# Optimization experiments

Measured on AMD Instinct MI355X. Metric: run time of the kernel, lower is better.

Reference implementation:

```python
import jax, jax.numpy as jnp
import numpy as np

NUM_HEADS = 8      # SD1.x UNet cross-attn heads at 64x64 block
NUM_PROMPTS = 4    # batch = 2*NUM_PROMPTS (uncond + cond CFG halves)


def setup_inputs() -> dict:
    key = jax.random.key(0)
    ks = jax.random.split(key, 8)
    B, T, C = 2 * NUM_PROMPTS, 4096, 320   # spatial tokens, inner dim
    S, D = 77, 768                          # CLIP text seq len / width
    return {
        "hidden_states": jax.random.normal(ks[0], (B, T, C), jnp.float32),
        "encoder_hidden_states": jax.random.normal(ks[1], (B, S, D), jnp.float32),
        "mapper": jax.random.uniform(ks[2], (NUM_PROMPTS - 1, S, S), jnp.float32),
        "Wq": jax.random.normal(ks[3], (C, C), jnp.float32) * 0.02,
        "Wk": jax.random.normal(ks[4], (D, C), jnp.float32) * 0.02,
        "Wv": jax.random.normal(ks[5], (D, C), jnp.float32) * 0.02,
        "Wo": jax.random.normal(ks[6], (C, C), jnp.float32) * 0.02,
        "bo": jnp.zeros((C,), jnp.float32),
    }


def reference(hidden_states, encoder_hidden_states, mapper, Wq, Wk, Wv, Wo, bo):
    B, T, C = hidden_states.shape
    S = encoder_hidden_states.shape[1]
    H = NUM_HEADS
    d = C // H
    scale = 1.0 / jnp.sqrt(jnp.asarray(d, hidden_states.dtype))

    # projections + head split (diffusers head_to_batch_dim layout)
    q = (hidden_states @ Wq).reshape(B, T, H, d)
    k = (encoder_hidden_states @ Wk).reshape(B, S, H, d)
    v = (encoder_hidden_states @ Wv).reshape(B, S, H, d)

    # full attention probabilities must be materialized for the P2P swap
    scores = jnp.einsum('bthd,bshd->bhts', q, k) * scale
    probs = jax.nn.softmax(scores, axis=-1)  # [B, H, T, S]

    # conditional (CFG) half: [P, H, T, S]; swap via mapper einsum (cross-attn,
    # cur_step < num_steps_cross branch of swap_attention_probs)
    half = B // 2
    uncond = probs[:half]
    cond = probs[half:]
    attn_base = cond[0]                                   # [H, T, S]
    replaced = jnp.einsum('htm,pme->phte', attn_base, mapper)  # [P-1, H, T, S]
    cond = jnp.concatenate([attn_base[None], replaced], axis=0)
    probs = jnp.concatenate([uncond, cond], axis=0)

    # value matmul + merge heads (batch_to_head_dim) + output projection
    out = jnp.einsum('bhts,bshd->bthd', probs, v).reshape(B, T, C)
    return out @ Wo + bo
```

## Files before the change

### kernel.cpp

```cpp
#include <hip/hip_runtime.h>
#include <hip/hip_bf16.h>

typedef unsigned short ushort;
typedef __attribute__((ext_vector_type(8))) short bf16x8;
typedef __attribute__((ext_vector_type(8))) unsigned short ushort8;
typedef __attribute__((ext_vector_type(4))) float f32x4;
typedef __attribute__((ext_vector_type(4))) float float4v;

__device__ __forceinline__ ushort f2bf(float f) {
    union { float f; unsigned u; } v; v.f = f;
    unsigned r = v.u + 0x7FFFu + ((v.u >> 16) & 1u);
    return (ushort)(r >> 16);
}
__device__ __forceinline__ float bf2f(ushort u) {
    union { unsigned u; float f; } v; v.u = ((unsigned)u) << 16;
    return v.f;
}

#define QF_SZ   (1280u * 8 * 2 * 512)
#define KF_SZ   (5u * 8 * 5 * 2 * 512)
#define VF_SZ   (5u * 8 * 3 * 3 * 512)
#define VPF_SZ  (3u * 8 * 3 * 3 * 512)
#define WOF_SZ  (10u * 2 * 10 * 512)

__global__ __launch_bounds__(256) void prep_k(
    const float* __restrict__ Wq, const float* __restrict__ Wk,
    const float* __restrict__ Wv, const float* __restrict__ Wo,
    ushort* __restrict__ Wq_t, ushort* __restrict__ Wk_t,
    ushort* __restrict__ Wv_t, ushort* __restrict__ Wo_t,
    ushort* __restrict__ Kf, ushort* __restrict__ Vf, ushort* __restrict__ VPf)
{
    int b = blockIdx.x;
    if (b >= 680) {
        const ushort8 z8 = {0,0,0,0,0,0,0,0};
        unsigned i = (b - 680) * 256 + threadIdx.x;
        if (i < KF_SZ / 8) ((ushort8*)Kf)[i] = z8;
        else if (i < (KF_SZ + VF_SZ) / 8) ((ushort8*)Vf)[i - KF_SZ / 8] = z8;
        else if (i < (KF_SZ + VF_SZ + VPF_SZ) / 8) ((ushort8*)VPf)[i - (KF_SZ + VF_SZ) / 8] = z8;
        return;
    }
    __shared__ ushort t[32][33];
    const float* src; ushort* dst; int K; int tb;
    if (b < 100)      { src = Wq; dst = Wq_t; K = 320; tb = b; }
    else if (b < 340) { src = Wk; dst = Wk_t; K = 768; tb = b - 100; }
    else if (b < 580) { src = Wv; dst = Wv_t; K = 768; tb = b - 340; }
    else              { src = Wo; dst = Wo_t; K = 320; tb = b - 580; }
    int tc = tb % 10, tr = tb / 10;
    int tx = threadIdx.x & 31, ty = threadIdx.x >> 5;
    #pragma unroll
    for (int p = 0; p < 4; ++p) {
        int k = tr * 32 + ty + p * 8, n = tc * 32 + tx;
        t[ty + p * 8][tx] = f2bf(src[(size_t)k * 320 + n]);
    }
    __syncthreads();
    #pragma unroll
    for (int p = 0; p < 4; ++p) {
        int n = tc * 32 + ty + p * 8, k = tr * 32 + tx;
        dst[(size_t)n * K + k] = t[tx][ty + p * 8];
    }
}

__global__ __launch_bounds__(256) void gemm_qkv(
    const float* __restrict__ A, const ushort* __restrict__ Wq_t,
    const float* __restrict__ E, const ushort* __restrict__ Wk_t,
    const ushort* __restrict__ Wv_t, const ushort* __restrict__ Wo_t,
    ushort* __restrict__ Qf, float* __restrict__ part, ushort* __restrict__ Wof)
{
    const int tid = threadIdx.x;
    const int bid = blockIdx.x;
    if (bid >= 480) {
        int i = (bid - 480) * 256 + tid;
        int g = i >> 6, l = i & 63;
        int kk = g / 20, half = (g / 10) & 1, f = g - (g / 10) * 10;
        int n = half * 160 + f * 16 + (l & 15);
        int k0 = kk * 32 + (l >> 4) * 8;
        *(ushort8*)(Wof + (size_t)g * 512 + l * 8) =
            *(const ushort8*)(Wo_t + (size_t)n * 320 + k0);
        return;
    }
    __shared__ ushort A_lds[2][64 * 40];
    __shared__ ushort B_lds[2][320 * 40];
    const int w = tid >> 6, l = tid & 63;
    const int c15 = l & 15, khi = (l >> 4) * 8;
    const int r = tid >> 2, p = (tid & 3) * 8;
    const int rbase = (l >> 4) * 4;
    f32x4 acc[4][5] = {};
    const ushort8 z8 = {0,0,0,0,0,0,0,0};

    if (bid < 160) {
        const int mtile = bid % 10, mat = (bid / 10) & 1, ks = bid / 20;
        const int m0 = mtile * 64, kk0 = ks * 96;
        const ushort* Bt = mat ? Wv_t : Wk_t;
        const int m = m0 + r;
        const bool live = (m < 616);
        const float* Abase = E + (size_t)(live ? m : 0) * 768 + p;
        float4v a0 = {0,0,0,0}, a1 = {0,0,0,0};
        ushort8 breg[5];
        if (live) { a0 = *(const float4v*)(Abase + kk0); a1 = *(const float4v*)(Abase + kk0 + 4); }
        #pragma unroll
        for (int i = 0; i < 5; ++i) {
            int idx = tid + i * 256; int n = idx >> 2, q = (idx & 3) * 8;
            breg[i] = *(const ushort8*)(Bt + (size_t)n * 768 + kk0 + q);
        }
        {
            ushort* d = &A_lds[0][r * 40 + p];
            d[0]=f2bf(a0.x); d[1]=f2bf(a0.y); d[2]=f2bf(a0.z); d[3]=f2bf(a0.w);
            d[4]=f2bf(a1.x); d[5]=f2bf(a1.y); d[6]=f2bf(a1.z); d[7]=f2bf(a1.w);
            #pragma unroll
            for (int i = 0; i < 5; ++i) {
                int idx = tid + i * 256; int n = idx >> 2, q = (idx & 3) * 8;
                *(ushort8*)&B_lds[0][n * 40 + q] = breg[i];
            }
        }
        __syncthreads();
        for (int k = 0; k < 3; ++k) {
            const int cur = k & 1;
            if (k < 2) {
                int kk = kk0 + (k + 1) * 32;
                if (live) { a0 = *(const float4v*)(Abase + kk); a1 = *(const float4v*)(Abase + kk + 4); }
                #pragma unroll
                for (int i = 0; i < 5; ++i) {
                    int idx = tid + i * 256; int n = idx >> 2, q = (idx & 3) * 8;
                    breg[i] = *(const ushort8*)(Bt + (size_t)n * 768 + kk + q);
                }
            }
            bf16x8 a[4];
            #pragma unroll
            for (int mf = 0; mf < 4; ++mf)
                a[mf] = *(const bf16x8*)&A_lds[cur][(mf * 16 + c15) * 40 + khi];
            #pragma unroll
            for (int f = 0; f < 5; ++f) {
                bf16x8 b = *(const bf16x8*)&B_lds[cur][(w * 80 + f * 16 + c15) * 40 + khi];
                #pragma unroll
                for (int mf = 0; mf < 4; ++mf)
                    acc[mf][f] = __builtin_amdgcn_mfma_f32_16x16x32_bf16(a[mf], b, acc[mf][f], 0, 0, 0);
            }
            if (k < 2) {
                const int nxt = cur ^ 1;
                ushort* d = &A_lds[nxt][r * 40 + p];
                d[0]=f2bf(a0.x); d[1]=f2bf(a0.y); d[2]=f2bf(a0.z); d[3]=f2bf(a0.w);
                d[4]=f2bf(a1.x); d[5]=f2bf(a1.y); d[6]=f2bf(a1.z); d[7]=f2bf(a1.w);
                #pragma unroll
                for (int i = 0; i < 5; ++i) {
                    int idx = tid + i * 256; int n = idx >> 2, q = (idx & 3) * 8;
                    *(ushort8*)&B_lds[nxt][n * 40 + q] = breg[i];
                }
                __syncthreads();
            }
        }
        float* dst = part + (size_t)(mat * 8 + ks) * 640 * 320;
        #pragma unroll
        for (int mf = 0; mf < 4; ++mf)
            #pragma unroll
            for (int f = 0; f < 5; ++f) {
                int col = w * 80 + f * 16 + c15;
                #pragma unroll
                for (int rr = 0; rr < 4; ++rr)
                    dst[(size_t)(m0 + mf * 16 + rbase + rr) * 320 + col] = acc[mf][f][rr];
            }
    } else {
        const int m0 = (bid - 160) * 64;
        const float* Abase = A + (size_t)(m0 + r) * 320 + p;
        float4v a0, a1; ushort8 breg[5];
        a0 = *(const float4v*)(Abase + 0);
        a1 = *(const float4v*)(Abase + 4);
        #pragma unroll
        for (int i = 0; i < 5; ++i) {
            int idx = tid + i * 256; int n = idx >> 2, q = (idx & 3) * 8;
            breg[i] = *(const ushort8*)(Wq_t + (size_t)n * 320 + q);
        }
        {
            ushort* d = &A_lds[0][r * 40 + p];
            d[0]=f2bf(a0.x); d[1]=f2bf(a0.y); d[2]=f2bf(a0.z); d[3]=f2bf(a0.w);
            d[4]=f2bf(a1.x); d[5]=f2bf(a1.y); d[6]=f2bf(a1.z); d[7]=f2bf(a1.w);
            #pragma unroll
            for (int i = 0; i < 5; ++i) {
                int idx = tid + i * 256; int n = idx >> 2, q = (idx & 3) * 8;
                *(ushort8*)&B_lds[0][n * 40 + q] = breg[i];
            }
        }
        __syncthreads();
        for (int k = 0; k < 10; ++k) {
            const int cur = k & 1;
            if (k < 9) {
                int kk = (k + 1) * 32;
                a0 = *(const float4v*)(Abase + kk);
                a1 = *(const float4v*)(Abase + kk + 4);
                #pragma unroll
                for (int i = 0; i < 5; ++i) {
                    int idx = tid + i * 256; int n = idx >> 2, q = (idx & 3) * 8;
                    breg[i] = *(const ushort8*)(Wq_t + (size_t)n * 320 + kk + q);
                }
            }
            bf16x8 a[4];
            #pragma unroll
            for (int mf = 0; mf < 4; ++mf)
                a[mf] = *(const bf16x8*)&A_lds[cur][(mf * 16 + c15) * 40 + khi];
            #pragma unroll
            for (int f = 0; f < 5; ++f) {
                bf16x8 b = *(const bf16x8*)&B_lds[cur][(w * 80 + f * 16 + c15) * 40 + khi];
                #pragma unroll
                for (int mf = 0; mf < 4; ++mf)
                    acc[mf][f] = __builtin_amdgcn_mfma_f32_16x16x32_bf16(a[mf], b, acc[mf][f], 0, 0, 0);
            }
            if (k < 9) {
                const int nxt = cur ^ 1;
                ushort* d = &A_lds[nxt][r * 40 + p];
                d[0]=f2bf(a0.x); d[1]=f2bf(a0.y); d[2]=f2bf(a0.z); d[3]=f2bf(a0.w);
                d[4]=f2bf(a1.x); d[5]=f2bf(a1.y); d[6]=f2bf(a1.z); d[7]=f2bf(a1.w);
                #pragma unroll
                for (int i = 0; i < 5; ++i) {
                    int idx = tid + i * 256; int n = idx >> 2, q = (idx & 3) * 8;
                    *(ushort8*)&B_lds[nxt][n * 40 + q] = breg[i];
                }
                __syncthreads();
            }
        }
        const int rg0 = m0 >> 4;
        for (int i = tid; i < 1536; i += 256) {
            int grp = i / 48;
            int lane16 = 16 + (i - grp * 48);
            int rg4 = grp >> 3, h = grp & 7;
            *(ushort8*)(Qf + ((size_t)((rg0 + rg4) * 8 + h) * 2 + 1) * 512 + lane16 * 8) = z8;
        }
        #pragma unroll
        for (int mf = 0; mf < 4; ++mf)
            #pragma unroll
            for (int f = 0; f < 5; ++f) {
                int col = w * 80 + f * 16 + c15;
                int h = col / 40, kd = col - h * 40;
                int kt = kd >> 5, chunk = (kd >> 3) & 3, elem = kd & 7;
                size_t base = ((size_t)((rg0 + mf) * 8 + h) * 2 + kt) * 512;
                #pragma unroll
                for (int rr = 0; rr < 4; ++rr) {
                    int lane = (rbase + rr) | (chunk << 4);
                    Qf[base + lane * 8 + elem] = f2bf(acc[mf][f][rr]);
                }
            }
    }
}

__global__ __launch_bounds__(256) void kv_reduce(
    const float* __restrict__ part, ushort* __restrict__ Kf,
    ushort* __restrict__ Vf, ushort* __restrict__ VVt)
{
    int idx = blockIdx.x * 256 + threadIdx.x;
    if (idx >= 616 * 320) return;
    int mat = blockIdx.y;
    int row = idx / 320, col = idx - row * 320;
    float s8 = 0.f;
    #pragma unroll
    for (int ks = 0; ks < 8; ++ks)
        s8 += part[((size_t)(mat * 8 + ks) * 640 + row) * 320 + col];
    ushort b = f2bf(s8);
    int bt = row / 77, s = row - bt * 77;
    int h = col / 40, kd = col - h * 40;
    if (mat == 0) {
        if (bt < 5) {
            int kt = kd >> 5, chunk = (kd >> 3) & 3;
            int lane = (s & 15) | (chunk << 4);
            Kf[((size_t)((bt * 8 + h) * 5 + (s >> 4)) * 2 + kt) * 512 + lane * 8 + (kd & 7)] = b;
        }
    } else {
        if (bt < 5) {
            int lane = (kd & 15) | (((s >> 3) & 3) << 4);
            Vf[(((size_t)(bt * 8 + h) * 3 + (kd >> 4)) * 3 + (s >> 5)) * 512 + lane * 8 + (s & 7)] = b;
        } else {
            VVt[((size_t)bt * 320 + col) * 80 + s] = b;
        }
    }
}

__global__ void vprime_k(const float* __restrict__ mapper, const ushort* __restrict__ VVt,
                         ushort* __restrict__ VPf)
{
    int pm = blockIdx.x;
    int p = pm / 77, m = pm - p * 77;
    __shared__ float mp[77];
    int tid = threadIdx.x;
    if (tid < 77) mp[tid] = mapper[(size_t)pm * 77 + tid];
    __syncthreads();
    const ushort* vrow = VVt + ((size_t)(5 + p) * 320 + tid) * 80;
    float acc = 0.f;
    for (int e = 0; e < 77; ++e) acc += mp[e] * bf2f(vrow[e]);
    int h = tid / 40, dc = tid - h * 40;
    int lane = (dc & 15) | (((m >> 3) & 3) << 4);
    VPf[(((size_t)(p * 8 + h) * 3 + (dc >> 4)) * 3 + (m >> 5)) * 512 + lane * 8 + (m & 7)] = f2bf(acc);
}

#define ATT_SCALE 0.15811388300841897f
__global__ __launch_bounds__(512, 4) void attn_out_k(
    const ushort* __restrict__ Qf, const ushort* __restrict__ Kf,
    const ushort* __restrict__ Vf, const ushort* __restrict__ VPf,
    const ushort* __restrict__ Wof, const float* __restrict__ bias,
    float* __restrict__ out)
{
    __shared__ __align__(16) ushort AO_lds[64 * 328];
    __shared__ __align__(16) ushort P_lds[8 * 16 * 104];

    const int tid = threadIdx.x;
    const int ww = tid >> 6, l = tid & 63;
    const int rg = ww & 3, half = ww >> 2;
    const int c15 = l & 15, hi4 = l >> 4;
    const int khi = hi4 * 8, rbase = hi4 * 4;
    const int bt = blockIdx.y, t0 = blockIdx.x * 64;
    const int qb = (bt < 5) ? bt : 4;
    const int rowgrp = qb * 256 + blockIdx.x * 4 + rg;
    const ushort* Vfb = (bt < 5) ? (Vf + (size_t)bt * (8 * 3 * 3 * 512))
                                 : (VPf + (size_t)(bt - 5) * (8 * 3 * 3 * 512));
    const ushort8 z8 = {0,0,0,0,0,0,0,0};
    ushort* Pw = P_lds + ww * (16 * 104);

    if (l < 48) {
        int r = l / 3, c = l - 3 * (l / 3);
        *(ushort8*)&Pw[r * 104 + 80 + c * 8] = z8;
    }

    for (int hh = 0; hh < 4; ++hh) {
        const int h = half * 4 + hh;

        bf16x8 qa0 = *(const bf16x8*)(Qf + ((size_t)(rowgrp * 8 + h) * 2 + 0) * 512 + l * 8);
        bf16x8 qa1 = *(const bf16x8*)(Qf + ((size_t)(rowgrp * 8 + h) * 2 + 1) * 512 + l * 8);
        f32x4 sacc[5] = {};
        #pragma unroll
        for (int f = 0; f < 5; ++f) {
            const ushort* kfb = Kf + ((size_t)((qb * 8 + h) * 5 + f) * 2) * 512 + l * 8;
            bf16x8 kb0 = *(const bf16x8*)(kfb);
            bf16x8 kb1 = *(const bf16x8*)(kfb + 512);
            sacc[f] = __builtin_amdgcn_mfma_f32_16x16x32_bf16(qa0, kb0, sacc[f], 0, 0, 0);
            sacc[f] = __builtin_amdgcn_mfma_f32_16x16x32_bf16(qa1, kb1, sacc[f], 0, 0, 0);
        }

        bf16x8 vreg[3][3];
        #pragma unroll
        for (int f = 0; f < 3; ++f)
            #pragma unroll
            for (int kt = 0; kt < 3; ++kt)
                vreg[f][kt] = *(const bf16x8*)(Vfb + (((size_t)(h * 3 + f) * 3 + kt)) * 512 + l * 8);

        float pv[5][4];
        #pragma unroll
        for (int r = 0; r < 4; ++r) {
            float sum = 0.f;
            #pragma unroll
            for (int f = 0; f < 5; ++f) {
                bool valid = (f < 4) || (c15 < 13);
                float e = valid ? __expf(sacc[f][r] * ATT_SCALE) : 0.f;
                pv[f][r] = e; sum += e;
            }
            #pragma unroll
            for (int d = 1; d < 16; d <<= 1) sum += __shfl_xor(sum, d);
            float inv = 1.f / sum;
            #pragma unroll
            for (int f = 0; f < 5; ++f) pv[f][r] *= inv;
        }

        #pragma unroll
        for (int r = 0; r < 4; ++r)
            #pragma unroll
            for (int f = 0; f < 5; ++f)
                Pw[(rbase + r) * 104 + f * 16 + c15] = f2bf(pv[f][r]);

        bf16x8 pa[3];
        #pragma unroll
        for (int kt = 0; kt < 3; ++kt)
            pa[kt] = *(const bf16x8*)&Pw[c15 * 104 + kt * 32 + khi];
        f32x4 oacc[3] = {};
        #pragma unroll
        for (int f = 0; f < 3; ++f)
            #pragma unroll
            for (int kt = 0; kt < 3; ++kt)
                oacc[f] = __builtin_amdgcn_mfma_f32_16x16x32_bf16(pa[kt], vreg[f][kt], oacc[f], 0, 0, 0);
        #pragma unroll
        for (int f = 0; f < 3; ++f) {
            int col = f * 16 + c15;
            if (col < 40) {
                #pragma unroll
                for (int r = 0; r < 4; ++r)
                    AO_lds[(rg * 16 + rbase + r) * 328 + h * 40 + col] = f2bf(oacc[f][r]);
            }
        }
    }
    __syncthreads();

    f32x4 acc[10] = {};
    for (int kk = 0; kk < 10; ++kk) {
        bf16x8 a = *(const bf16x8*)&AO_lds[(rg * 16 + c15) * 328 + kk * 32 + khi];
        const ushort* wb = Wof + (size_t)((kk * 2 + half) * 10) * 512 + l * 8;
        #pragma unroll
        for (int f = 0; f < 10; ++f) {
            bf16x8 b = *(const bf16x8*)(wb + (size_t)f * 512);
            acc[f] = __builtin_amdgcn_mfma_f32_16x16x32_bf16(a, b, acc[f], 0, 0, 0);
        }
    }

    const int cb = half * 160;
    #pragma unroll
    for (int f = 0; f < 10; ++f) {
        int col = cb + f * 16 + c15;
        #pragma unroll
        for (int rr = 0; rr < 4; ++rr)
            out[(size_t)(bt * 4096 + t0 + rg * 16 + rbase + rr) * 320 + col]
                = acc[f][rr] + bias[col];
    }
}

extern "C" void kernel_launch(void* const* d_in, const int* in_sizes, int n_in,
                              void* d_out, int out_size, void* d_ws, size_t ws_size,
                              hipStream_t stream) {
    (void)in_sizes; (void)n_in; (void)out_size; (void)ws_size;
    const float* hs     = (const float*)d_in[0];
    const float* ehs    = (const float*)d_in[1];
    const float* mapper = (const float*)d_in[2];
    const float* Wq     = (const float*)d_in[3];
    const float* Wk     = (const float*)d_in[4];
    const float* Wv     = (const float*)d_in[5];
    const float* Wo     = (const float*)d_in[6];
    const float* bo     = (const float*)d_in[7];
    float* out = (float*)d_out;

    ushort* ws   = (ushort*)d_ws;
    ushort* Wq_t = ws;
    ushort* Wk_t = Wq_t + 320 * 320;
    ushort* Wv_t = Wk_t + 320 * 768;
    ushort* Wo_t = Wv_t + 320 * 768;
    ushort* Wof  = Wo_t + 320 * 320;
    ushort* Qfb  = Wof + WOF_SZ;
    ushort* Kfb  = Qfb + QF_SZ;
    ushort* Vfb  = Kfb + KF_SZ;
    ushort* VPfb = Vfb + VF_SZ;
    ushort* VVt  = VPfb + VPF_SZ;
    float*  part = (float*)(VVt + 8 * 320 * 80);

    prep_k<<<1069, 256, 0, stream>>>(Wq, Wk, Wv, Wo, Wq_t, Wk_t, Wv_t, Wo_t,
                                     Kfb, Vfb, VPfb);
    gemm_qkv<<<530, 256, 0, stream>>>(hs, Wq_t, ehs, Wk_t, Wv_t, Wo_t, Qfb, part, Wof);
    kv_reduce<<<dim3(770, 2), 256, 0, stream>>>(part, Kfb, Vfb, VVt);
    vprime_k<<<231, 320, 0, stream>>>(mapper, VVt, VPfb);
    attn_out_k<<<dim3(64, 8), 512, 0, stream>>>(Qfb, Kfb, Vfb, VPfb, Wof, bo, out);
}
```

Measured before the change: 68.54 us.

## Fuse Q projection into attention kernel, dropping the global Q buffer

The Q projection moves out of the standalone QKV GEMM and into the attention/output kernel. Each block loads its 64 hidden-state rows, converts them to bf16 in LDS, multiplies by a pre-fragmented Wq (Wqf, built alongside Wof), and reads per-head Q fragments straight from LDS. This removes the large write and re-read of Qf through global memory and shrinks the first GEMM launch to K/V only. The cost is recomputing Q for the three cond batches that share batch 4's queries, plus an extra LDS pass and barrier in the attention kernel.

```diff
diff --git a/kernel.cpp b/kernel.cpp
--- a/kernel.cpp
+++ b/kernel.cpp
@@ -17,11 +17,10 @@
     return v.f;
 }
 
-#define QF_SZ   (1280u * 8 * 2 * 512)
 #define KF_SZ   (5u * 8 * 5 * 2 * 512)
 #define VF_SZ   (5u * 8 * 3 * 3 * 512)
 #define VPF_SZ  (3u * 8 * 3 * 3 * 512)
-#define WOF_SZ  (10u * 2 * 10 * 512)
+#define WF_SZ   (10u * 2 * 10 * 512)
 
 __global__ __launch_bounds__(256) void prep_k(
     const float* __restrict__ Wq, const float* __restrict__ Wk,
@@ -60,22 +59,25 @@
     }
 }
 
-__global__ __launch_bounds__(256) void gemm_qkv(
-    const float* __restrict__ A, const ushort* __restrict__ Wq_t,
+__global__ __launch_bounds__(256) void gemm_kv(
     const float* __restrict__ E, const ushort* __restrict__ Wk_t,
-    const ushort* __restrict__ Wv_t, const ushort* __restrict__ Wo_t,
-    ushort* __restrict__ Qf, float* __restrict__ part, ushort* __restrict__ Wof)
+    const ushort* __restrict__ Wv_t, const ushort* __restrict__ Wq_t,
+    const ushort* __restrict__ Wo_t,
+    float* __restrict__ part, ushort* __restrict__ Wof, ushort* __restrict__ Wqf)
 {
     const int tid = threadIdx.x;
     const int bid = blockIdx.x;
-    if (bid >= 480) {
-        int i = (bid - 480) * 256 + tid;
+    if (bid >= 160) {
+        int i = (bid - 160) * 256 + tid;
+        const ushort* src; ushort* dst;
+        if (i < 12800) { src = Wo_t; dst = Wof; }
+        else           { src = Wq_t; dst = Wqf; i -= 12800; }
         int g = i >> 6, l = i & 63;
-        int kk = g / 20, half = (g / 10) & 1, f = g - (g / 10) * 10;
+        int kk = g / 20, half = (g / 10) & 1, f = g % 10;
         int n = half * 160 + f * 16 + (l & 15);
         int k0 = kk * 32 + (l >> 4) * 8;
-        *(ushort8*)(Wof + (size_t)g * 512 + l * 8) =
-            *(const ushort8*)(Wo_t + (size_t)n * 320 + k0);
+        *(ushort8*)(dst + (size_t)g * 512 + l * 8) =
+            *(const ushort8*)(src + (size_t)n * 320 + k0);
         return;
     }
     __shared__ ushort A_lds[2][64 * 40];
@@ -85,159 +87,77 @@
     const int r = tid >> 2, p = (tid & 3) * 8;
     const int rbase = (l >> 4) * 4;
     f32x4 acc[4][5] = {};
-    const ushort8 z8 = {0,0,0,0,0,0,0,0};
-
-    if (bid < 160) {
-        const int mtile = bid % 10, mat = (bid / 10) & 1, ks = bid / 20;
-        const int m0 = mtile * 64, kk0 = ks * 96;
-        const ushort* Bt = mat ? Wv_t : Wk_t;
-        const int m = m0 + r;
-        const bool live = (m < 616);
-        const float* Abase = E + (size_t)(live ? m : 0) * 768 + p;
-        float4v a0 = {0,0,0,0}, a1 = {0,0,0,0};
-        ushort8 breg[5];
-        if (live) { a0 = *(const float4v*)(Abase + kk0); a1 = *(const float4v*)(Abase + kk0 + 4); }
+
+    const int mtile = bid % 10, mat = (bid / 10) & 1, ks = bid / 20;
+    const int m0 = mtile * 64, kk0 = ks * 96;
+    const ushort* Bt = mat ? Wv_t : Wk_t;
+    const int m = m0 + r;
+    const bool live = (m < 616);
+    const float* Abase = E + (size_t)(live ? m : 0) * 768 + p;
+    float4v a0 = {0,0,0,0}, a1 = {0,0,0,0};
+    ushort8 breg[5];
+    if (live) { a0 = *(const float4v*)(Abase + kk0); a1 = *(const float4v*)(Abase + kk0 + 4); }
+    #pragma unroll
+    for (int i = 0; i < 5; ++i) {
+        int idx = tid + i * 256; int n = idx >> 2, q = (idx & 3) * 8;
+        breg[i] = *(const ushort8*)(Bt + (size_t)n * 768 + kk0 + q);
+    }
+    {
+        ushort* d = &A_lds[0][r * 40 + p];
+        d[0]=f2bf(a0.x); d[1]=f2bf(a0.y); d[2]=f2bf(a0.z); d[3]=f2bf(a0.w);
+        d[4]=f2bf(a1.x); d[5]=f2bf(a1.y); d[6]=f2bf(a1.z); d[7]=f2bf(a1.w);
         #pragma unroll
         for (int i = 0; i < 5; ++i) {
             int idx = tid + i * 256; int n = idx >> 2, q = (idx & 3) * 8;
-            breg[i] = *(const ushort8*)(Bt + (size_t)n * 768 + kk0 + q);
-        }
-        {
-            ushort* d = &A_lds[0][r * 40 + p];
+            *(ushort8*)&B_lds[0][n * 40 + q] = breg[i];
+        }
+    }
+    __syncthreads();
+    for (int k = 0; k < 3; ++k) {
+        const int cur = k & 1;
+        if (k < 2) {
+            int kk = kk0 + (k + 1) * 32;
+            if (live) { a0 = *(const float4v*)(Abase + kk); a1 = *(const float4v*)(Abase + kk + 4); }
+            #pragma unroll
+            for (int i = 0; i < 5; ++i) {
+                int idx = tid + i * 256; int n = idx >> 2, q = (idx & 3) * 8;
+                breg[i] = *(const ushort8*)(Bt + (size_t)n * 768 + kk + q);
+            }
+        }
+        bf16x8 a[4];
+        #pragma unroll
+        for (int mf = 0; mf < 4; ++mf)
+            a[mf] = *(const bf16x8*)&A_lds[cur][(mf * 16 + c15) * 40 + khi];
+        #pragma unroll
+        for (int f = 0; f < 5; ++f) {
+            bf16x8 b = *(const bf16x8*)&B_lds[cur][(w * 80 + f * 16 + c15) * 40 + khi];
+            #pragma unroll
+            for (int mf = 0; mf < 4; ++mf)
+                acc[mf][f] = __builtin_amdgcn_mfma_f32_16x16x32_bf16(a[mf], b, acc[mf][f], 0, 0, 0);
+        }
+        if (k < 2) {
+            const int nxt = cur ^ 1;
+            ushort* d = &A_lds[nxt][r * 40 + p];
             d[0]=f2bf(a0.x); d[1]=f2bf(a0.y); d[2]=f2bf(a0.z); d[3]=f2bf(a0.w);
             d[4]=f2bf(a1.x); d[5]=f2bf(a1.y); d[6]=f2bf(a1.z); d[7]=f2bf(a1.w);
             #pragma unroll
             for (int i = 0; i < 5; ++i) {
                 int idx = tid + i * 256; int n = idx >> 2, q = (idx & 3) * 8;
-                *(ushort8*)&B_lds[0][n * 40 + q] = breg[i];
+                *(ushort8*)&B_lds[nxt][n * 40 + q] = breg[i];
             }
-        }
-        __syncthreads();
-        for (int k = 0; k < 3; ++k) {
-            const int cur = k & 1;
-            if (k < 2) {
-                int kk = kk0 + (k + 1) * 32;
-                if (live) { a0 = *(const float4v*)(Abase + kk); a1 = *(const float4v*)(Abase + kk + 4); }
-                #pragma unroll
-                for (int i = 0; i < 5; ++i) {
-                    int idx = tid + i * 256; int n = idx >> 2, q = (idx & 3) * 8;
-                    breg[i] = *(const ushort8*)(Bt + (size_t)n * 768 + kk + q);
-                }
-            }
-            bf16x8 a[4];
-            #pragma unroll
-            for (int mf = 0; mf < 4; ++mf)
-                a[mf] = *(const bf16x8*)&A_lds[cur][(mf * 16 + c15) * 40 + khi];
-            #pragma unroll
-            for (int f = 0; f < 5; ++f) {
-                bf16x8 b = *(const bf16x8*)&B_lds[cur][(w * 80 + f * 16 + c15) * 40 + khi];
-                #pragma unroll
-                for (int mf = 0; mf < 4; ++mf)
-                    acc[mf][f] = __builtin_amdgcn_mfma_f32_16x16x32_bf16(a[mf], b, acc[mf][f], 0, 0, 0);
-            }
-            if (k < 2) {
-                const int nxt = cur ^ 1;
-                ushort* d = &A_lds[nxt][r * 40 + p];
-                d[0]=f2bf(a0.x); d[1]=f2bf(a0.y); d[2]=f2bf(a0.z); d[3]=f2bf(a0.w);
-                d[4]=f2bf(a1.x); d[5]=f2bf(a1.y); d[6]=f2bf(a1.z); d[7]=f2bf(a1.w);
-                #pragma unroll
-                for (int i = 0; i < 5; ++i) {
-                    int idx = tid + i * 256; int n = idx >> 2, q = (idx & 3) * 8;
-                    *(ushort8*)&B_lds[nxt][n * 40 + q] = breg[i];
-                }
-                __syncthreads();
-            }
-        }
-        float* dst = part + (size_t)(mat * 8 + ks) * 640 * 320;
-        #pragma unroll
-        for (int mf = 0; mf < 4; ++mf)
-            #pragma unroll
-            for (int f = 0; f < 5; ++f) {
-                int col = w * 80 + f * 16 + c15;
-                #pragma unroll
-                for (int rr = 0; rr < 4; ++rr)
-                    dst[(size_t)(m0 + mf * 16 + rbase + rr) * 320 + col] = acc[mf][f][rr];
-            }
-    } else {
-        const int m0 = (bid - 160) * 64;
-        const float* Abase = A + (size_t)(m0 + r) * 320 + p;
-        float4v a0, a1; ushort8 breg[5];
-        a0 = *(const float4v*)(Abase + 0);
-        a1 = *(const float4v*)(Abase + 4);
-        #pragma unroll
-        for (int i = 0; i < 5; ++i) {
-            int idx = tid + i * 256; int n = idx >> 2, q = (idx & 3) * 8;
-            breg[i] = *(const ushort8*)(Wq_t + (size_t)n * 320 + q);
-        }
-        {
-            ushort* d = &A_lds[0][r * 40 + p];
-            d[0]=f2bf(a0.x); d[1]=f2bf(a0.y); d[2]=f2bf(a0.z); d[3]=f2bf(a0.w);
-            d[4]=f2bf(a1.x); d[5]=f2bf(a1.y); d[6]=f2bf(a1.z); d[7]=f2bf(a1.w);
-            #pragma unroll
-            for (int i = 0; i < 5; ++i) {
-                int idx = tid + i * 256; int n = idx >> 2, q = (idx & 3) * 8;
-                *(ushort8*)&B_lds[0][n * 40 + q] = breg[i];
-            }
-        }
-        __syncthreads();
-        for (int k = 0; k < 10; ++k) {
-            const int cur = k & 1;
-            if (k < 9) {
-                int kk = (k + 1) * 32;
-                a0 = *(const float4v*)(Abase + kk);
-                a1 = *(const float4v*)(Abase + kk + 4);
-                #pragma unroll
-                for (int i = 0; i < 5; ++i) {
-                    int idx = tid + i * 256; int n = idx >> 2, q = (idx & 3) * 8;
-                    breg[i] = *(const ushort8*)(Wq_t + (size_t)n * 320 + kk + q);
-                }
-            }
-            bf16x8 a[4];
-            #pragma unroll
-            for (int mf = 0; mf < 4; ++mf)
-                a[mf] = *(const bf16x8*)&A_lds[cur][(mf * 16 + c15) * 40 + khi];
-            #pragma unroll
-            for (int f = 0; f < 5; ++f) {
-                bf16x8 b = *(const bf16x8*)&B_lds[cur][(w * 80 + f * 16 + c15) * 40 + khi];
-                #pragma unroll
-                for (int mf = 0; mf < 4; ++mf)
-                    acc[mf][f] = __builtin_amdgcn_mfma_f32_16x16x32_bf16(a[mf], b, acc[mf][f], 0, 0, 0);
-            }
-            if (k < 9) {
-                const int nxt = cur ^ 1;
-                ushort* d = &A_lds[nxt][r * 40 + p];
-                d[0]=f2bf(a0.x); d[1]=f2bf(a0.y); d[2]=f2bf(a0.z); d[3]=f2bf(a0.w);
-                d[4]=f2bf(a1.x); d[5]=f2bf(a1.y); d[6]=f2bf(a1.z); d[7]=f2bf(a1.w);
-                #pragma unroll
-                for (int i = 0; i < 5; ++i) {
-                    int idx = tid + i * 256; int n = idx >> 2, q = (idx & 3) * 8;
-                    *(ushort8*)&B_lds[nxt][n * 40 + q] = breg[i];
-                }
-                __syncthreads();
-            }
-        }
-        const int rg0 = m0 >> 4;
-        for (int i = tid; i < 1536; i += 256) {
-            int grp = i / 48;
-            int lane16 = 16 + (i - grp * 48);
-            int rg4 = grp >> 3, h = grp & 7;
-            *(ushort8*)(Qf + ((size_t)((rg0 + rg4) * 8 + h) * 2 + 1) * 512 + lane16 * 8) = z8;
-        }
-        #pragma unroll
-        for (int mf = 0; mf < 4; ++mf)
-            #pragma unroll
-            for (int f = 0; f < 5; ++f) {
-                int col = w * 80 + f * 16 + c15;
-                int h = col / 40, kd = col - h * 40;
-                int kt = kd >> 5, chunk = (kd >> 3) & 3, elem = kd & 7;
-                size_t base = ((size_t)((rg0 + mf) * 8 + h) * 2 + kt) * 512;
-                #pragma unroll
-                for (int rr = 0; rr < 4; ++rr) {
-                    int lane = (rbase + rr) | (chunk << 4);
-                    Qf[base + lane * 8 + elem] = f2bf(acc[mf][f][rr]);
-                }
-            }
-    }
+            __syncthreads();
+        }
+    }
+    float* dst = part + (size_t)(mat * 8 + ks) * 640 * 320;
+    #pragma unroll
+    for (int mf = 0; mf < 4; ++mf)
+        #pragma unroll
+        for (int f = 0; f < 5; ++f) {
+            int col = w * 80 + f * 16 + c15;
+            #pragma unroll
+            for (int rr = 0; rr < 4; ++rr)
+                dst[(size_t)(m0 + mf * 16 + rbase + rr) * 320 + col] = acc[mf][f][rr];
+        }
 }
 
 __global__ __launch_bounds__(256) void kv_reduce(
@@ -290,10 +210,10 @@
 
 #define ATT_SCALE 0.15811388300841897f
 __global__ __launch_bounds__(512, 4) void attn_out_k(
-    const ushort* __restrict__ Qf, const ushort* __restrict__ Kf,
-    const ushort* __restrict__ Vf, const ushort* __restrict__ VPf,
-    const ushort* __restrict__ Wof, const float* __restrict__ bias,
-    float* __restrict__ out)
+    const float* __restrict__ hs, const ushort* __restrict__ Wqf,
+    const ushort* __restrict__ Kf, const ushort* __restrict__ Vf,
+    const ushort* __restrict__ VPf, const ushort* __restrict__ Wof,
+    const float* __restrict__ bias, float* __restrict__ out)
 {
     __shared__ __align__(16) ushort AO_lds[64 * 328];
     __shared__ __align__(16) ushort P_lds[8 * 16 * 104];
@@ -305,7 +225,6 @@
     const int khi = hi4 * 8, rbase = hi4 * 4;
     const int bt = blockIdx.y, t0 = blockIdx.x * 64;
     const int qb = (bt < 5) ? bt : 4;
-    const int rowgrp = qb * 256 + blockIdx.x * 4 + rg;
     const ushort* Vfb = (bt < 5) ? (Vf + (size_t)bt * (8 * 3 * 3 * 512))
                                  : (VPf + (size_t)(bt - 5) * (8 * 3 * 3 * 512));
     const ushort8 z8 = {0,0,0,0,0,0,0,0};
@@ -316,11 +235,44 @@
         *(ushort8*)&Pw[r * 104 + 80 + c * 8] = z8;
     }
 
+    for (int i = tid; i < 2560; i += 512) {
+        int r = i / 40, cc = i - (i / 40) * 40;
+        const float4v* s = (const float4v*)(hs + (size_t)(qb * 4096 + t0 + r) * 320 + cc * 8);
+        float4v x0 = s[0], x1 = s[1];
+        ushort* d = &AO_lds[r * 328 + cc * 8];
+        d[0]=f2bf(x0.x); d[1]=f2bf(x0.y); d[2]=f2bf(x0.z); d[3]=f2bf(x0.w);
+        d[4]=f2bf(x1.x); d[5]=f2bf(x1.y); d[6]=f2bf(x1.z); d[7]=f2bf(x1.w);
+    }
+    __syncthreads();
+
+    const int cb = half * 160;
+    {
+        f32x4 qacc[10] = {};
+        for (int kk = 0; kk < 10; ++kk) {
+            bf16x8 a = *(const bf16x8*)&AO_lds[(rg * 16 + c15) * 328 + kk * 32 + khi];
+            const ushort* wb = Wqf + (size_t)((kk * 2 + half) * 10) * 512 + l * 8;
+            #pragma unroll
+            for (int f = 0; f < 10; ++f)
+                qacc[f] = __builtin_amdgcn_mfma_f32_16x16x32_bf16(
+                    a, *(const bf16x8*)(wb + (size_t)f * 512), qacc[f], 0, 0, 0);
+        }
+        __syncthreads();
+        #pragma unroll
+        for (int f = 0; f < 10; ++f) {
+            int col = cb + f * 16 + c15;
+            #pragma unroll
+            for (int rr = 0; rr < 4; ++rr)
+                AO_lds[(rg * 16 + rbase + rr) * 328 + col] = f2bf(qacc[f][rr]);
+        }
+    }
+
     for (int hh = 0; hh < 4; ++hh) {
         const int h = half * 4 + hh;
 
-        bf16x8 qa0 = *(const bf16x8*)(Qf + ((size_t)(rowgrp * 8 + h) * 2 + 0) * 512 + l * 8);
-        bf16x8 qa1 = *(const bf16x8*)(Qf + ((size_t)(rowgrp * 8 + h) * 2 + 1) * 512 + l * 8);
+        bf16x8 qa0 = *(const bf16x8*)&AO_lds[(rg * 16 + c15) * 328 + h * 40 + khi];
+        bf16x8 qa1 = {0,0,0,0,0,0,0,0};
+        if (hi4 == 0) qa1 = *(const bf16x8*)&AO_lds[(rg * 16 + c15) * 328 + h * 40 + 32];
+
         f32x4 sacc[5] = {};
         #pragma unroll
         for (int f = 0; f < 5; ++f) {
@@ -371,6 +323,7 @@
             #pragma unroll
             for (int kt = 0; kt < 3; ++kt)
                 oacc[f] = __builtin_amdgcn_mfma_f32_16x16x32_bf16(pa[kt], vreg[f][kt], oacc[f], 0, 0, 0);
+
         #pragma unroll
         for (int f = 0; f < 3; ++f) {
             int col = f * 16 + c15;
@@ -394,7 +347,6 @@
         }
     }
 
-    const int cb = half * 160;
     #pragma unroll
     for (int f = 0; f < 10; ++f) {
         int col = cb + f * 16 + c15;
@@ -425,8 +377,8 @@
     ushort* Wv_t = Wk_t + 320 * 768;
     ushort* Wo_t = Wv_t + 320 * 768;
     ushort* Wof  = Wo_t + 320 * 320;
-    ushort* Qfb  = Wof + WOF_SZ;
-    ushort* Kfb  = Qfb + QF_SZ;
+    ushort* Wqf  = Wof + WF_SZ;
+    ushort* Kfb  = Wqf + WF_SZ;
     ushort* Vfb  = Kfb + KF_SZ;
     ushort* VPfb = Vfb + VF_SZ;
     ushort* VVt  = VPfb + VPF_SZ;
@@ -434,8 +386,8 @@
 
     prep_k<<<1069, 256, 0, stream>>>(Wq, Wk, Wv, Wo, Wq_t, Wk_t, Wv_t, Wo_t,
                                      Kfb, Vfb, VPfb);
-    gemm_qkv<<<530, 256, 0, stream>>>(hs, Wq_t, ehs, Wk_t, Wv_t, Wo_t, Qfb, part, Wof);
+    gemm_kv<<<260, 256, 0, stream>>>(ehs, Wk_t, Wv_t, Wq_t, Wo_t, part, Wof, Wqf);
     kv_reduce<<<dim3(770, 2), 256, 0, stream>>>(part, Kfb, Vfb, VVt);
     vprime_k<<<231, 320, 0, stream>>>(mapper, VVt, VPfb);
-    attn_out_k<<<dim3(64, 8), 512, 0, stream>>>(Qfb, Kfb, Vfb, VPfb, Wof, bo, out);
-}
+    attn_out_k<<<dim3(64, 8), 512, 0, stream>>>(hs, Wqf, Kfb, Vfb, VPfb, Wof, bo, out);
+}
```

Measured after the change: 74.44 us. +8.6%, slower.

## Assign one head per wave in attention and stage Wo tiles in LDS

Applied to the files above, without the earlier changes.

The attention phase now gives each of the 8 waves one head and loops over the block's 4 row groups, so each wave loads its K fragments into registers once and reuses them. Previously each wave looped over 4 heads for a single row group. V fragments are now loaded inside each output tile step. In the output projection, each 32-wide k-slice of packed Wo is loaded cooperatively into LDS, reusing the P buffer, and all waves read it from there instead of each wave fetching from global memory. This cuts redundant global and L2 traffic, at the cost of two barriers per k-step and V reloads for every row group.

```diff
diff --git a/kernel.cpp b/kernel.cpp
--- a/kernel.cpp
+++ b/kernel.cpp
@@ -21,7 +21,7 @@
 #define KF_SZ   (5u * 8 * 5 * 2 * 512)
 #define VF_SZ   (5u * 8 * 3 * 3 * 512)
 #define VPF_SZ  (3u * 8 * 3 * 3 * 512)
-#define WOF_SZ  (10u * 2 * 10 * 512)
+#define WF_SZ   (10u * 2 * 10 * 512)
 
 __global__ __launch_bounds__(256) void prep_k(
     const float* __restrict__ Wq, const float* __restrict__ Wk,
@@ -71,7 +71,7 @@
     if (bid >= 480) {
         int i = (bid - 480) * 256 + tid;
         int g = i >> 6, l = i & 63;
-        int kk = g / 20, half = (g / 10) & 1, f = g - (g / 10) * 10;
+        int kk = g / 20, half = (g / 10) & 1, f = g % 10;
         int n = half * 160 + f * 16 + (l & 15);
         int k0 = kk * 32 + (l >> 4) * 8;
         *(ushort8*)(Wof + (size_t)g * 512 + l * 8) =
@@ -297,15 +297,15 @@
 {
     __shared__ __align__(16) ushort AO_lds[64 * 328];
     __shared__ __align__(16) ushort P_lds[8 * 16 * 104];
+    ushort* W_lds = P_lds;
 
     const int tid = threadIdx.x;
     const int ww = tid >> 6, l = tid & 63;
-    const int rg = ww & 3, half = ww >> 2;
     const int c15 = l & 15, hi4 = l >> 4;
     const int khi = hi4 * 8, rbase = hi4 * 4;
-    const int bt = blockIdx.y, t0 = blockIdx.x * 64;
+    const int bt = blockIdx.y;
     const int qb = (bt < 5) ? bt : 4;
-    const int rowgrp = qb * 256 + blockIdx.x * 4 + rg;
+    const int h = ww;
     const ushort* Vfb = (bt < 5) ? (Vf + (size_t)bt * (8 * 3 * 3 * 512))
                                  : (VPf + (size_t)(bt - 5) * (8 * 3 * 3 * 512));
     const ushort8 z8 = {0,0,0,0,0,0,0,0};
@@ -316,27 +316,26 @@
         *(ushort8*)&Pw[r * 104 + 80 + c * 8] = z8;
     }
 
-    for (int hh = 0; hh < 4; ++hh) {
-        const int h = half * 4 + hh;
+    bf16x8 kreg[5][2];
+    #pragma unroll
+    for (int f = 0; f < 5; ++f) {
+        const ushort* kfb = Kf + ((size_t)((qb * 8 + h) * 5 + f) * 2) * 512 + l * 8;
+        kreg[f][0] = *(const bf16x8*)(kfb);
+        kreg[f][1] = *(const bf16x8*)(kfb + 512);
+    }
+
+    for (int rg4 = 0; rg4 < 4; ++rg4) {
+        const int rowgrp = qb * 256 + blockIdx.x * 4 + rg4;
 
         bf16x8 qa0 = *(const bf16x8*)(Qf + ((size_t)(rowgrp * 8 + h) * 2 + 0) * 512 + l * 8);
         bf16x8 qa1 = *(const bf16x8*)(Qf + ((size_t)(rowgrp * 8 + h) * 2 + 1) * 512 + l * 8);
+
         f32x4 sacc[5] = {};
         #pragma unroll
         for (int f = 0; f < 5; ++f) {
-            const ushort* kfb = Kf + ((size_t)((qb * 8 + h) * 5 + f) * 2) * 512 + l * 8;
-            bf16x8 kb0 = *(const bf16x8*)(kfb);
-            bf16x8 kb1 = *(const bf16x8*)(kfb + 512);
-            sacc[f] = __builtin_amdgcn_mfma_f32_16x16x32_bf16(qa0, kb0, sacc[f], 0, 0, 0);
-            sacc[f] = __builtin_amdgcn_mfma_f32_16x16x32_bf16(qa1, kb1, sacc[f], 0, 0, 0);
-        }
-
-        bf16x8 vreg[3][3];
-        #pragma unroll
-        for (int f = 0; f < 3; ++f)
-            #pragma unroll
-            for (int kt = 0; kt < 3; ++kt)
-                vreg[f][kt] = *(const bf16x8*)(Vfb + (((size_t)(h * 3 + f) * 3 + kt)) * 512 + l * 8);
+            sacc[f] = __builtin_amdgcn_mfma_f32_16x16x32_bf16(qa0, kreg[f][0], sacc[f], 0, 0, 0);
+            sacc[f] = __builtin_amdgcn_mfma_f32_16x16x32_bf16(qa1, kreg[f][1], sacc[f], 0, 0, 0);
+        }
 
         float pv[5][4];
         #pragma unroll
@@ -365,36 +364,53 @@
         #pragma unroll
         for (int kt = 0; kt < 3; ++kt)
             pa[kt] = *(const bf16x8*)&Pw[c15 * 104 + kt * 32 + khi];
-        f32x4 oacc[3] = {};
-        #pragma unroll
-        for (int f = 0; f < 3; ++f)
-            #pragma unroll
-            for (int kt = 0; kt < 3; ++kt)
-                oacc[f] = __builtin_amdgcn_mfma_f32_16x16x32_bf16(pa[kt], vreg[f][kt], oacc[f], 0, 0, 0);
+        f32x4 oacc[3];
+        #pragma unroll
+        for (int f = 0; f < 3; ++f) {
+            bf16x8 v0 = *(const bf16x8*)(Vfb + (((size_t)(h * 3 + f) * 3 + 0)) * 512 + l * 8);
+            bf16x8 v1 = *(const bf16x8*)(Vfb + (((size_t)(h * 3 + f) * 3 + 1)) * 512 + l * 8);
+            bf16x8 v2 = *(const bf16x8*)(Vfb + (((size_t)(h * 3 + f) * 3 + 2)) * 512 + l * 8);
+            f32x4 o = {};
+            o = __builtin_amdgcn_mfma_f32_16x16x32_bf16(pa[0], v0, o, 0, 0, 0);
+            o = __builtin_amdgcn_mfma_f32_16x16x32_bf16(pa[1], v1, o, 0, 0, 0);
+            o = __builtin_amdgcn_mfma_f32_16x16x32_bf16(pa[2], v2, o, 0, 0, 0);
+            oacc[f] = o;
+        }
+
         #pragma unroll
         for (int f = 0; f < 3; ++f) {
             int col = f * 16 + c15;
             if (col < 40) {
                 #pragma unroll
                 for (int r = 0; r < 4; ++r)
-                    AO_lds[(rg * 16 + rbase + r) * 328 + h * 40 + col] = f2bf(oacc[f][r]);
+                    AO_lds[(rg4 * 16 + rbase + r) * 328 + h * 40 + col] = f2bf(oacc[f][r]);
             }
         }
     }
     __syncthreads();
 
+    const int rg = ww & 3, half = ww >> 2;
+    const int cb = half * 160;
     f32x4 acc[10] = {};
     for (int kk = 0; kk < 10; ++kk) {
+        const ushort* wsrc = Wof + (size_t)kk * 10240;
+        {
+            int c0 = tid, c1 = tid + 512, c2 = tid + 1024;
+            *(ushort8*)&W_lds[c0 * 8] = *(const ushort8*)(wsrc + c0 * 8);
+            *(ushort8*)&W_lds[c1 * 8] = *(const ushort8*)(wsrc + c1 * 8);
+            if (c2 < 1280) *(ushort8*)&W_lds[c2 * 8] = *(const ushort8*)(wsrc + c2 * 8);
+        }
+        __syncthreads();
         bf16x8 a = *(const bf16x8*)&AO_lds[(rg * 16 + c15) * 328 + kk * 32 + khi];
-        const ushort* wb = Wof + (size_t)((kk * 2 + half) * 10) * 512 + l * 8;
         #pragma unroll
         for (int f = 0; f < 10; ++f) {
-            bf16x8 b = *(const bf16x8*)(wb + (size_t)f * 512);
+            bf16x8 b = *(const bf16x8*)&W_lds[(half * 10 + f) * 512 + l * 8];
             acc[f] = __builtin_amdgcn_mfma_f32_16x16x32_bf16(a, b, acc[f], 0, 0, 0);
         }
-    }
-
-    const int cb = half * 160;
+        if (kk < 9) __syncthreads();
+    }
+
+    const int t0 = blockIdx.x * 64;
     #pragma unroll
     for (int f = 0; f < 10; ++f) {
         int col = cb + f * 16 + c15;
@@ -425,7 +441,7 @@
     ushort* Wv_t = Wk_t + 320 * 768;
     ushort* Wo_t = Wv_t + 320 * 768;
     ushort* Wof  = Wo_t + 320 * 320;
-    ushort* Qfb  = Wof + WOF_SZ;
+    ushort* Qfb  = Wof + WF_SZ;
     ushort* Kfb  = Qfb + QF_SZ;
     ushort* Vfb  = Kfb + KF_SZ;
     ushort* VPfb = Vfb + VF_SZ;
```

New measurement: 65.47 us, median of 2. 4.5% less time.
